# Optimization experiments

Measured on AMD Instinct MI355X. Metric: run time of the kernel, lower is better.

Reference implementation:

```python
import jax, jax.numpy as jnp
import numpy as np
from jax.scipy.special import logsumexp

# K particles, J proposal candidates, N taxa, R merges done, T current subtrees,
# S sites, A alphabet, D embedding dim
K, J, N, R, T, S, A, D = 128, 4, 64, 32, 32, 256, 4, 64
PRIOR_BL = 0.1       # expected branch length under exponential prior
TEMPERATURE = 1.0


def _gather_nodes(arr, idx):
    # arr: (Z, t, ...); idx: (Z,) -> (Z, ...)  (per-row gather, gather_K)
    i = idx.reshape((-1,) + (1,) * (arr.ndim - 1))
    return jnp.take_along_axis(arr, i, axis=1)[:, 0]


def _replace_with_merged(arr, idx1, idx2, new_val):
    # remove nodes idx1, idx2 from each row (keeping order) and append merged node
    t = arr.shape[1]
    pos = jnp.arange(t)
    removed = (pos[None, :] == idx1[:, None]) | (pos[None, :] == idx2[:, None])
    order = jnp.argsort(removed.astype(jnp.int32), axis=1, stable=True)
    kept = order[:, : t - 2]
    ki = kept.reshape(kept.shape + (1,) * (arr.ndim - 2))
    kept_vals = jnp.take_along_axis(arr, ki, axis=1)
    return jnp.concatenate([kept_vals, new_val[:, None]], axis=1)


def _hash_tree(h1, h2):
    # order-invariant int32 hash combine (wraps on overflow, as intended)
    mn = jnp.minimum(h1, h2)
    mx = jnp.maximum(h1, h2)
    return (mn * 1000003 + mx) * 40503 + 2531011


def _q_matrix(emb_ZxD, W_q):
    # GTR-style rate matrix from merged-node embedding (site-independent decoder)
    logits = (emb_ZxD @ W_q).reshape(-1, A, A)
    off = jax.nn.softplus(logits) * (1.0 - jnp.eye(A, dtype=logits.dtype))
    return off - jnp.eye(A, dtype=logits.dtype) * off.sum(-1, keepdims=True)


def setup_inputs() -> dict:
    key = jax.random.key(0)
    ks = jax.random.split(key, 20)
    merge1_indexes_Kxr = jax.random.randint(ks[0], (K, R), 0, N).astype(jnp.int32)
    merge2_indexes_Kxr = jax.random.randint(ks[1], (K, R), 0, N).astype(jnp.int32)
    branch1_lengths_Kxr = jax.random.uniform(ks[2], (K, R)) * 0.2 + 1e-3
    branch2_lengths_Kxr = jax.random.uniform(ks[3], (K, R)) * 0.2 + 1e-3
    embeddings_KxrxD = jax.random.normal(ks[4], (K, R, D))
    # leaf counts per subtree, summing to N per particle
    lc_row = jnp.concatenate([jnp.full((T // 2,), 1, jnp.int32), jnp.full((T - T // 2,), 3, jnp.int32)])
    leaf_counts_Kxt = jnp.tile(lc_row[None], (K, 1))
    hashes_Kxt = jax.random.randint(ks[5], (K, T), 0, 2 ** 30).astype(jnp.int32)
    embeddings_KxtxD = jax.random.normal(ks[6], (K, T, D))
    log_felsensteins_KxtxSxA = -jax.random.uniform(ks[7], (K, T, S, A)) * 3.0
    log_pi_K = -jax.random.uniform(ks[8], (K,)) * 100.0
    indexes_K = jax.random.randint(ks[9], (K,), 0, K).astype(jnp.int32)
    # proposal outputs (stand-in for the learned proposal): idx1 != idx2
    idx1_KxJ = jax.random.randint(ks[10], (K, J), 0, T).astype(jnp.int32)
    off = jax.random.randint(ks[11], (K, J), 1, T).astype(jnp.int32)
    idx2_KxJ = (idx1_KxJ + off) % T
    branch1_KxJ = jax.random.uniform(ks[12], (K, J)) * 0.2 + 1e-3
    branch2_KxJ = jax.random.uniform(ks[13], (K, J)) * 0.2 + 1e-3
    embedding_KxJxD = jax.random.normal(ks[14], (K, J, D))
    log_v_plus_KxJ = jnp.full((K, J), np.log(T * (T - 1) / 2.0), jnp.float32)
    gumbel_KxJ = jax.random.gumbel(ks[15], (K, J))
    W_q = jax.random.normal(ks[16], (D, A * A)) * 0.05
    W_stat = jax.random.normal(ks[17], (D, A)) * 0.05
    vals = np.zeros(2 * N, dtype=np.float64)
    for i in range(2, 2 * N):
        vals[i] = vals[i - 2] + np.log(i)
    log_double_factorials_2N = jnp.asarray(vals, jnp.float32)
    return {
        'indexes_K': indexes_K,
        'merge1_indexes_Kxr': merge1_indexes_Kxr,
        'merge2_indexes_Kxr': merge2_indexes_Kxr,
        'branch1_lengths_Kxr': branch1_lengths_Kxr,
        'branch2_lengths_Kxr': branch2_lengths_Kxr,
        'embeddings_KxrxD': embeddings_KxrxD,
        'leaf_counts_Kxt': leaf_counts_Kxt,
        'hashes_Kxt': hashes_Kxt,
        'embeddings_KxtxD': embeddings_KxtxD,
        'log_felsensteins_KxtxSxA': log_felsensteins_KxtxSxA,
        'log_pi_K': log_pi_K,
        'idx1_KxJ': idx1_KxJ,
        'idx2_KxJ': idx2_KxJ,
        'branch1_KxJ': branch1_KxJ,
        'branch2_KxJ': branch2_KxJ,
        'embedding_KxJxD': embedding_KxJxD,
        'log_v_plus_KxJ': log_v_plus_KxJ,
        'gumbel_KxJ': gumbel_KxJ,
        'W_q': W_q,
        'W_stat': W_stat,
        'log_double_factorials_2N': log_double_factorials_2N,
    }


def reference(indexes_K, merge1_indexes_Kxr, merge2_indexes_Kxr,
              branch1_lengths_Kxr, branch2_lengths_Kxr, embeddings_KxrxD,
              leaf_counts_Kxt, hashes_Kxt, embeddings_KxtxD,
              log_felsensteins_KxtxSxA, log_pi_K,
              idx1_KxJ, idx2_KxJ, branch1_KxJ, branch2_KxJ,
              embedding_KxJxD, log_v_plus_KxJ, gumbel_KxJ,
              W_q, W_stat, log_double_factorials_2N):
    # ---- ancestor resampling gather (ms[...][indexes_K]) ----
    g = lambda a: a[indexes_K]
    merge1_Kxr = g(merge1_indexes_Kxr); merge2_Kxr = g(merge2_indexes_Kxr)
    b1_Kxr = g(branch1_lengths_Kxr); b2_Kxr = g(branch2_lengths_Kxr)
    emb_KxrxD = g(embeddings_KxrxD)
    lc_Kxt = g(leaf_counts_Kxt); h_Kxt = g(hashes_Kxt)
    emb_KxtxD = g(embeddings_KxtxD)
    lf_KxtxSxA = g(log_felsensteins_KxtxSxA)
    logpi_K = g(log_pi_K)
    # ---- flatten proposal to Z = K*J (hash_trick=False: Z = K*J, no dedup) ----
    Z = K * J
    rep = lambda a: jnp.repeat(a, J, axis=0)  # K_to_Z
    idx1_Z = idx1_KxJ.reshape(Z); idx2_Z = idx2_KxJ.reshape(Z)
    branch1_Z = branch1_KxJ.reshape(Z); branch2_Z = branch2_KxJ.reshape(Z)
    emb_ZxD = embedding_KxJxD.reshape(Z, D)
    log_v_plus_Z = log_v_plus_KxJ.reshape(Z)
    merge1_Z = rep(merge1_Kxr); merge2_Z = rep(merge2_Kxr)
    b1_Z = rep(b1_Kxr); b2_Z = rep(b2_Kxr)
    embr_Z = rep(emb_KxrxD)
    lc_Z = rep(lc_Kxt); h_Z = rep(h_Kxt)
    embt_Z = rep(emb_KxtxD)
    lf_Z = rep(lf_KxtxSxA)
    logpi_Z = rep(logpi_K)
    # ---- append candidate branches ----
    b1_all = jnp.concatenate([b1_Z, branch1_Z[:, None]], axis=1)  # Z x (R+1)
    b2_all = jnp.concatenate([b2_Z, branch2_Z[:, None]], axis=1)
    # ---- merge step ----
    new_lc = _gather_nodes(lc_Z, idx1_Z) + _gather_nodes(lc_Z, idx2_Z)
    new_h = _hash_tree(_gather_nodes(h_Z, idx1_Z), _gather_nodes(h_Z, idx2_Z))
    lc_new = _replace_with_merged(lc_Z, idx1_Z, idx2_Z, new_lc)      # Z x (T-1)
    h_new = _replace_with_merged(h_Z, idx1_Z, idx2_Z, new_h)
    embt_new = _replace_with_merged(embt_Z, idx1_Z, idx2_Z, emb_ZxD)
    # ---- Felsenstein pruning update ----
    Q = _q_matrix(emb_ZxD, W_q)                                      # Z x A x A
    expm = jax.scipy.linalg.expm
    P1 = jax.vmap(expm)(Q * branch1_Z[:, None, None])
    P2 = jax.vmap(expm)(Q * branch2_Z[:, None, None])
    logP1 = jnp.log(jnp.clip(P1, 1e-30))
    logP2 = jnp.log(jnp.clip(P2, 1e-30))
    lf1 = _gather_nodes(lf_Z, idx1_Z)  # Z x S x A
    lf2 = _gather_nodes(lf_Z, idx2_Z)
    new_lf = (logsumexp(logP1[:, None, :, :] + lf1[:, :, None, :], axis=-1)
              + logsumexp(logP2[:, None, :, :] + lf2[:, :, None, :], axis=-1))
    lf_new = _replace_with_merged(lf_Z, idx1_Z, idx2_Z, new_lf)      # Z x (T-1) x S x A
    # ---- stationary probs per node & log pi ----
    log_stat = jax.nn.log_softmax(embt_new @ W_stat, axis=-1)        # Z x (T-1) x A
    ll_nodes = logsumexp(lf_new + log_stat[:, :, None, :], axis=-1).sum(-1)  # Z x (T-1)
    log_lik_Z = ll_nodes.sum(-1)
    rate = 1.0 / PRIOR_BL
    log_branch_prior = ((jnp.log(rate) - rate * b1_all).sum(-1)
                        + (jnp.log(rate) - rate * b2_all).sum(-1))
    df_idx = jnp.clip(2 * lc_new - 3, 0, 2 * N - 1)
    log_topo = -log_double_factorials_2N[df_idx].sum(-1)
    log_pi_new_Z = log_lik_Z + log_branch_prior + log_topo
    log_v_minus_Z = jnp.log(jnp.sum(lc_new > 1, axis=-1).astype(jnp.float32))
    # ---- weights & sub-resampling ----
    log_w_Z = log_pi_new_Z - logpi_Z + log_v_minus_Z - log_v_plus_Z
    log_w_KxJ = log_w_Z.reshape(K, J)
    log_weight_K = logsumexp(log_w_KxJ, axis=1) - jnp.log(float(J))
    sub_idx_K = jnp.argmax(log_w_KxJ / TEMPERATURE + gumbel_KxJ, axis=1)  # Gumbel-max = Categorical sample
    sel = jnp.arange(K) * J + sub_idx_K
    gs = lambda a: a[sel]
    merge1_out = jnp.concatenate([gs(merge1_Z), gs(idx1_Z)[:, None]], axis=1)
    merge2_out = jnp.concatenate([gs(merge2_Z), gs(idx2_Z)[:, None]], axis=1)
    embr_out = jnp.concatenate([gs(embr_Z), gs(emb_ZxD)[:, None, :]], axis=1)
    return (merge1_out, merge2_out, gs(b1_all), gs(b2_all), embr_out,
            gs(lc_new), gs(h_new), gs(embt_new), gs(lf_new),
            gs(log_pi_new_Z), log_weight_K, gs(log_lik_Z))
```

## Files before the change

### kernel.cpp

```cpp
#include <hip/hip_runtime.h>
#include <math.h>

constexpr int K_ = 128, J_ = 4, R_ = 32, T_ = 32, S_ = 256, A_ = 4, D_ = 64;
constexpr int NDF_ = 128;
constexpr float RATE_ = 10.0f;

constexpr int OFF_M1   = 0;
constexpr int OFF_M2   = OFF_M1 + K_ * 33;
constexpr int OFF_B1   = OFF_M2 + K_ * 33;
constexpr int OFF_B2   = OFF_B1 + K_ * 33;
constexpr int OFF_EMBR = OFF_B2 + K_ * 33;
constexpr int OFF_LC   = OFF_EMBR + K_ * 33 * D_;
constexpr int OFF_H    = OFF_LC + K_ * 31;
constexpr int OFF_EMBT = OFF_H + K_ * 31;
constexpr int OFF_LF   = OFF_EMBT + K_ * 31 * D_;
constexpr int OFF_LPN  = OFF_LF + K_ * 31 * S_ * A_;
constexpr int OFF_LW   = OFF_LPN + K_;
constexpr int OFF_LL   = OFF_LW + K_;

constexpr int WS_NODE  = 0;
constexpr int WS_NEWLL = WS_NODE + K_ * T_;
constexpr int WS_LOGP  = WS_NEWLL + K_ * J_;

__device__ inline float lse4f(float a, float b, float c, float d) {
    float m = fmaxf(fmaxf(a, b), fmaxf(c, d));
    return m + __logf(__expf(a - m) + __expf(b - m) + __expf(c - m) + __expf(d - m));
}

__global__ __launch_bounds__(256) void k_compute(
    const int* __restrict__ indexes, const float* __restrict__ embt,
    const float* __restrict__ lf, const float* __restrict__ Wstat,
    const float* __restrict__ Wq, const int* __restrict__ idx1_KJ,
    const int* __restrict__ idx2_KJ, const float* __restrict__ br1_KJ,
    const float* __restrict__ br2_KJ, const float* __restrict__ emb_KJD,
    float* __restrict__ ws) {
    int grp = blockIdx.x;
    int k = blockIdx.y;
    int tid = threadIdx.x, w = tid >> 6, lane = tid & 63;
    int src = indexes[k];

    if (grp < 8) {
        int t = grp * 4 + w;
        float e = embt[(src * T_ + t) * D_ + lane];
        const float4 w4 = *(const float4*)&Wstat[lane * 4];
        float g0 = e * w4.x, g1 = e * w4.y, g2 = e * w4.z, g3 = e * w4.w;
#pragma unroll
        for (int m = 32; m; m >>= 1) {
            g0 += __shfl_xor(g0, m, 64);
            g1 += __shfl_xor(g1, m, 64);
            g2 += __shfl_xor(g2, m, 64);
            g3 += __shfl_xor(g3, m, 64);
        }
        float lse = lse4f(g0, g1, g2, g3);
        float ls0 = g0 - lse, ls1 = g1 - lse, ls2 = g2 - lse, ls3 = g3 - lse;
        const float4* fr = (const float4*)&lf[(size_t)(src * T_ + t) * S_ * A_];
        double acc = 0.0;
#pragma unroll
        for (int s4 = 0; s4 < 4; ++s4) {
            float4 f = fr[s4 * 64 + lane];
            acc += (double)lse4f(f.x + ls0, f.y + ls1, f.z + ls2, f.w + ls3);
        }
#pragma unroll
        for (int m = 32; m; m >>= 1) acc += __shfl_xor(acc, m, 64);
        if (lane == 0) ws[WS_NODE + k * T_ + t] = (float)acc;
    } else {
        int z = k * J_ + w;
        int i1 = idx1_KJ[z], i2 = idx2_KJ[z];

        float emb_d = emb_KJD[z * D_ + lane];
        float lg[20];
        const float4* wqr = (const float4*)&Wq[lane * 16];
        float4 q0 = wqr[0], q1 = wqr[1], q2 = wqr[2], q3 = wqr[3];
        lg[0] = emb_d * q0.x;  lg[1] = emb_d * q0.y;  lg[2] = emb_d * q0.z;  lg[3] = emb_d * q0.w;
        lg[4] = emb_d * q1.x;  lg[5] = emb_d * q1.y;  lg[6] = emb_d * q1.z;  lg[7] = emb_d * q1.w;
        lg[8] = emb_d * q2.x;  lg[9] = emb_d * q2.y;  lg[10] = emb_d * q2.z; lg[11] = emb_d * q2.w;
        lg[12] = emb_d * q3.x; lg[13] = emb_d * q3.y; lg[14] = emb_d * q3.z; lg[15] = emb_d * q3.w;
        const float4 ws4 = *(const float4*)&Wstat[lane * 4];
        lg[16] = emb_d * ws4.x; lg[17] = emb_d * ws4.y; lg[18] = emb_d * ws4.z; lg[19] = emb_d * ws4.w;
#pragma unroll
        for (int m = 32; m; m >>= 1) {
#pragma unroll
            for (int p = 0; p < 20; ++p) lg[p] += __shfl_xor(lg[p], m, 64);
        }

        float lseS = lse4f(lg[16], lg[17], lg[18], lg[19]);
        float ls0 = lg[16] - lseS, ls1 = lg[17] - lseS, ls2 = lg[18] - lseS, ls3 = lg[19] - lseS;

        float lv[4] = {0.f, 0.f, 0.f, 0.f};
        if (lane < 8) {
            int h = lane >> 2, r = lane & 3, base = h * 4;
            float q[16];
#pragma unroll
            for (int i = 0; i < 4; ++i) {
                float rs = 0.f;
#pragma unroll
                for (int j = 0; j < 4; ++j) {
                    if (i != j) {
                        float x = lg[i * 4 + j];
                        float sp = (x > 15.f) ? x : log1pf(__expf(x));
                        q[i * 4 + j] = sp;
                        rs += sp;
                    }
                }
                q[i * 4 + i] = -rs;
            }
            float br = (h == 0) ? br1_KJ[z] : br2_KJ[z];
            float c = br * (1.f / 64.f);
#pragma unroll
            for (int e2 = 0; e2 < 16; ++e2) q[e2] *= c;
            float trow[4], arow[4];
#pragma unroll
            for (int j = 0; j < 4; ++j) { trow[j] = (j == r) ? 1.f : 0.f; arow[j] = trow[j]; }
            const float inv_n[11] = {0.f, 1.f, 0.5f, 1.f / 3.f, 0.25f, 0.2f,
                                     1.f / 6.f, 1.f / 7.f, 0.125f, 1.f / 9.f, 0.1f};
#pragma unroll
            for (int n = 1; n <= 10; ++n) {
                float nt[4];
#pragma unroll
                for (int j = 0; j < 4; ++j)
                    nt[j] = (trow[0] * q[0 * 4 + j] + trow[1] * q[1 * 4 + j] +
                             trow[2] * q[2 * 4 + j] + trow[3] * q[3 * 4 + j]) * inv_n[n];
#pragma unroll
                for (int j = 0; j < 4; ++j) { trow[j] = nt[j]; arow[j] += nt[j]; }
            }
#pragma unroll
            for (int sq = 0; sq < 6; ++sq) {
                float nrow[4];
#pragma unroll
                for (int j = 0; j < 4; ++j) {
                    float aj = arow[j];
                    nrow[j] = arow[0] * __shfl(aj, base + 0, 64)
                            + arow[1] * __shfl(aj, base + 1, 64)
                            + arow[2] * __shfl(aj, base + 2, 64)
                            + arow[3] * __shfl(aj, base + 3, 64);
                }
#pragma unroll
                for (int j = 0; j < 4; ++j) arow[j] = nrow[j];
            }
#pragma unroll
            for (int j = 0; j < 4; ++j) {
                lv[j] = __logf(fmaxf(arow[j], 1e-30f));
                ws[WS_LOGP + z * 32 + h * 16 + r * 4 + j] = lv[j];
            }
        }
        float p1[16], p2[16];
#pragma unroll
        for (int r = 0; r < 4; ++r) {
#pragma unroll
            for (int j = 0; j < 4; ++j) {
                p1[r * 4 + j] = __shfl(lv[j], r, 64);
                p2[r * 4 + j] = __shfl(lv[j], 4 + r, 64);
            }
        }
        const float4* f1p = (const float4*)&lf[(size_t)(src * T_ + i1) * S_ * A_];
        const float4* f2p = (const float4*)&lf[(size_t)(src * T_ + i2) * S_ * A_];
        double acc = 0.0;
#pragma unroll
        for (int s4 = 0; s4 < 4; ++s4) {
            float4 f = f1p[s4 * 64 + lane];
            float4 f2v = f2p[s4 * 64 + lane];
            float nlf[4];
#pragma unroll
            for (int a = 0; a < 4; ++a) {
                float t1 = lse4f(p1[a * 4 + 0] + f.x, p1[a * 4 + 1] + f.y,
                                 p1[a * 4 + 2] + f.z, p1[a * 4 + 3] + f.w);
                float t2 = lse4f(p2[a * 4 + 0] + f2v.x, p2[a * 4 + 1] + f2v.y,
                                 p2[a * 4 + 2] + f2v.z, p2[a * 4 + 3] + f2v.w);
                nlf[a] = t1 + t2;
            }
            acc += (double)lse4f(nlf[0] + ls0, nlf[1] + ls1, nlf[2] + ls2, nlf[3] + ls3);
        }
#pragma unroll
        for (int m = 32; m; m >>= 1) acc += __shfl_xor(acc, m, 64);
        if (lane == 0) ws[WS_NEWLL + z] = (float)acc;
    }
}

__global__ __launch_bounds__(256) void k_out(
    const int* __restrict__ indexes, const int* __restrict__ m1_Kr,
    const int* __restrict__ m2_Kr, const float* __restrict__ b1_Kr,
    const float* __restrict__ b2_Kr, const float* __restrict__ embr,
    const int* __restrict__ lc_Kt, const int* __restrict__ h_Kt,
    const float* __restrict__ embt, const float* __restrict__ lf,
    const float* __restrict__ logpi_K, const int* __restrict__ idx1_KJ,
    const int* __restrict__ idx2_KJ, const float* __restrict__ br1_KJ,
    const float* __restrict__ br2_KJ, const float* __restrict__ emb_KJD,
    const float* __restrict__ logvp_KJ, const float* __restrict__ gumbel_KJ,
    const float* __restrict__ ldf, const float* __restrict__ ws,
    float* __restrict__ out) {
    int grp = blockIdx.x;
    int k = blockIdx.y;
    int tid = threadIdx.x, lane = tid & 63;
    int src = indexes[k];

    double nll = 0.0, topo = 0.0, sb1 = 0.0, sb2 = 0.0;
    int cnt = 0;
    if (lane < T_) {
        nll = (double)ws[WS_NODE + k * T_ + lane];
        int lc = lc_Kt[src * T_ + lane];
        int di = 2 * lc - 3; di = max(0, min(NDF_ - 1, di));
        topo = (double)ldf[di];
        cnt = (lc > 1) ? 1 : 0;
        sb1 = (double)b1_Kr[src * R_ + lane];
        sb2 = (double)b2_Kr[src * R_ + lane];
    }
#pragma unroll
    for (int m = 32; m; m >>= 1) {
        nll += __shfl_xor(nll, m, 64);
        topo += __shfl_xor(topo, m, 64);
        sb1 += __shfl_xor(sb1, m, 64);
        sb2 += __shfl_xor(sb2, m, 64);
        cnt += __shfl_xor(cnt, m, 64);
    }
    double total_ll = nll, base_topo = -topo;
    const double lr = log(10.0);

    double lwj = 0.0, lpnj = 0.0, llikj = 0.0, scorej = -1.0e300;
    if (lane < J_) {
        int j = lane, z = k * J_ + j;
        int i1 = idx1_KJ[z], i2 = idx2_KJ[z];
        int lc1 = lc_Kt[src * T_ + i1], lc2 = lc_Kt[src * T_ + i2];
        int nlc = lc1 + lc2;
        double loglik = total_ll - (double)ws[WS_NODE + k * T_ + i1]
                      - (double)ws[WS_NODE + k * T_ + i2] + (double)ws[WS_NEWLL + z];
        double lbp = 66.0 * lr
                   - (double)RATE_ * (sb1 + (double)br1_KJ[z] + sb2 + (double)br2_KJ[z]);
        int d1 = max(0, min(NDF_ - 1, 2 * lc1 - 3));
        int d2 = max(0, min(NDF_ - 1, 2 * lc2 - 3));
        int dn = max(0, min(NDF_ - 1, 2 * nlc - 3));
        double lt = base_topo + (double)ldf[d1] + (double)ldf[d2] - (double)ldf[dn];
        int cntj = cnt - ((lc1 > 1) ? 1 : 0) - ((lc2 > 1) ? 1 : 0) + 1;
        double lvm = log((double)cntj);
        lpnj = loglik + lbp + lt;
        llikj = loglik;
        lwj = lpnj - (double)logpi_K[src] + lvm - (double)logvp_KJ[z];
        scorej = lwj + (double)gumbel_KJ[z];
    }
    double lw0 = __shfl(lwj, 0, 64), lw1 = __shfl(lwj, 1, 64);
    double lw2 = __shfl(lwj, 2, 64), lw3 = __shfl(lwj, 3, 64);
    double sc0 = __shfl(scorej, 0, 64), sc1 = __shfl(scorej, 1, 64);
    double sc2 = __shfl(scorej, 2, 64), sc3 = __shfl(scorej, 3, 64);
    int best = 0;
    double bv = sc0;
    if (sc1 > bv) { bv = sc1; best = 1; }
    if (sc2 > bv) { bv = sc2; best = 2; }
    if (sc3 > bv) { bv = sc3; best = 3; }
    int zs = k * J_ + best;
    int si1 = idx1_KJ[zs], si2 = idx2_KJ[zs];
    int mn = min(si1, si2), mx = max(si1, si2);

    if (grp < 8) {
        __shared__ float sP[32];
        if (grp == 7) {
            if (tid < 32) sP[tid] = ws[WS_LOGP + zs * 32 + tid];
            __syncthreads();
        }
#pragma unroll
        for (int rr = 0; rr < 4; ++rr) {
            int row = grp * 4 + rr;
            if (row >= 31) break;
            if (row < 30) {
                int st = row;
                if (st >= mn) ++st;
                if (st >= mx) ++st;
                const float4 v = *(const float4*)&lf[((size_t)(src * T_ + st) * S_ + tid) * A_];
                *(float4*)&out[OFF_LF + ((size_t)(k * 31 + row) * S_ + tid) * A_] = v;
            } else {
                float P1[16], P2[16];
#pragma unroll
                for (int i = 0; i < 16; ++i) { P1[i] = sP[i]; P2[i] = sP[16 + i]; }
                const float4 f1 = *(const float4*)&lf[((size_t)(src * T_ + si1) * S_ + tid) * A_];
                const float4 f2 = *(const float4*)&lf[((size_t)(src * T_ + si2) * S_ + tid) * A_];
                float4 o4;
#pragma unroll
                for (int a = 0; a < 4; ++a) {
                    float t1 = lse4f(P1[a * 4 + 0] + f1.x, P1[a * 4 + 1] + f1.y,
                                     P1[a * 4 + 2] + f1.z, P1[a * 4 + 3] + f1.w);
                    float t2 = lse4f(P2[a * 4 + 0] + f2.x, P2[a * 4 + 1] + f2.y,
                                     P2[a * 4 + 2] + f2.z, P2[a * 4 + 3] + f2.w);
                    ((float*)&o4)[a] = t1 + t2;
                }
                *(float4*)&out[OFF_LF + ((size_t)(k * 31 + 30) * S_ + tid) * A_] = o4;
            }
        }
    } else {
        if (tid == 0) {
            double m = fmax(fmax(lw0, lw1), fmax(lw2, lw3));
            double ssum = exp(lw0 - m) + exp(lw1 - m) + exp(lw2 - m) + exp(lw3 - m);
            double logw = m + log(ssum) - log((double)J_);
            out[OFF_LW + k] = (float)logw;
        }
        double lpn_b = __shfl(lpnj, best, 64);
        double llik_b = __shfl(llikj, best, 64);
        if (tid == 0) {
            out[OFF_LPN + k] = (float)lpn_b;
            out[OFF_LL + k] = (float)llik_b;
        }
        for (int i = tid; i < 33; i += 256) {
            float v1, v2, fb1, fb2;
            if (i < 32) {
                v1 = (float)m1_Kr[src * R_ + i];
                v2 = (float)m2_Kr[src * R_ + i];
                fb1 = b1_Kr[src * R_ + i];
                fb2 = b2_Kr[src * R_ + i];
            } else {
                v1 = (float)si1; v2 = (float)si2;
                fb1 = br1_KJ[zs]; fb2 = br2_KJ[zs];
            }
            out[OFF_M1 + k * 33 + i] = v1;
            out[OFF_M2 + k * 33 + i] = v2;
            out[OFF_B1 + k * 33 + i] = fb1;
            out[OFF_B2 + k * 33 + i] = fb2;
        }
        for (int i = tid; i < 31; i += 256) {
            int lcv, hv;
            if (i < 30) {
                int st = i;
                if (st >= mn) ++st;
                if (st >= mx) ++st;
                lcv = lc_Kt[src * T_ + st];
                hv = h_Kt[src * T_ + st];
            } else {
                lcv = lc_Kt[src * T_ + si1] + lc_Kt[src * T_ + si2];
                int h1 = h_Kt[src * T_ + si1], h2 = h_Kt[src * T_ + si2];
                int hmn = min(h1, h2), hmx = max(h1, h2);
                unsigned int u = ((unsigned int)hmn * 1000003u + (unsigned int)hmx) * 40503u
                                 + 2531011u;
                hv = (int)u;
            }
            out[OFF_LC + k * 31 + i] = (float)lcv;
            out[OFF_H + k * 31 + i] = (float)hv;
        }
        for (int i = tid; i < 33 * 16; i += 256) {
            int r = i >> 4, c = i & 15;
            float4 v = (r < 32) ? *(const float4*)&embr[(src * R_ + r) * D_ + c * 4]
                                : *(const float4*)&emb_KJD[zs * D_ + c * 4];
            *(float4*)&out[OFF_EMBR + k * 33 * D_ + i * 4] = v;
        }
        for (int i = tid; i < 31 * 16; i += 256) {
            int t = i >> 4, c = i & 15;
            float4 v;
            if (t < 30) {
                int st = t;
                if (st >= mn) ++st;
                if (st >= mx) ++st;
                v = *(const float4*)&embt[(src * T_ + st) * D_ + c * 4];
            } else {
                v = *(const float4*)&emb_KJD[zs * D_ + c * 4];
            }
            *(float4*)&out[OFF_EMBT + k * 31 * D_ + i * 4] = v;
        }
    }
}

extern "C" void kernel_launch(void* const* d_in, const int* in_sizes, int n_in,
                              void* d_out, int out_size, void* d_ws, size_t ws_size,
                              hipStream_t stream) {
    const int* indexes   = (const int*)d_in[0];
    const int* m1_Kr     = (const int*)d_in[1];
    const int* m2_Kr     = (const int*)d_in[2];
    const float* b1_Kr   = (const float*)d_in[3];
    const float* b2_Kr   = (const float*)d_in[4];
    const float* embr    = (const float*)d_in[5];
    const int* lc_Kt     = (const int*)d_in[6];
    const int* h_Kt      = (const int*)d_in[7];
    const float* embt    = (const float*)d_in[8];
    const float* lf      = (const float*)d_in[9];
    const float* logpi_K = (const float*)d_in[10];
    const int* idx1_KJ   = (const int*)d_in[11];
    const int* idx2_KJ   = (const int*)d_in[12];
    const float* br1_KJ  = (const float*)d_in[13];
    const float* br2_KJ  = (const float*)d_in[14];
    const float* emb_KJD = (const float*)d_in[15];
    const float* logvp_KJ = (const float*)d_in[16];
    const float* gumbel_KJ = (const float*)d_in[17];
    const float* Wq      = (const float*)d_in[18];
    const float* Wstat   = (const float*)d_in[19];
    const float* ldf     = (const float*)d_in[20];
    float* out = (float*)d_out;
    float* ws = (float*)d_ws;

    k_compute<<<dim3(9, K_), 256, 0, stream>>>(indexes, embt, lf, Wstat, Wq,
                                               idx1_KJ, idx2_KJ, br1_KJ, br2_KJ,
                                               emb_KJD, ws);
    k_out<<<dim3(9, K_), 256, 0, stream>>>(indexes, m1_Kr, m2_Kr, b1_Kr, b2_Kr,
                                           embr, lc_Kt, h_Kt, embt, lf, logpi_K,
                                           idx1_KJ, idx2_KJ, br1_KJ, br2_KJ,
                                           emb_KJD, logvp_KJ, gumbel_KJ, ldf,
                                           ws, out);
}
```

Before: 132.0 us.

## Fuse compute and output kernels with per-particle atomic counter barrier

Merges the compute and output kernels into one launch. The 9 blocks of each particle synchronise through an atomic counter in workspace that a memset clears before the launch. This removes the kernel boundary and second launch, but adds a spin-wait barrier that relies on all blocks of a particle being co-resident. It also adds a memset operation and shifts the workspace offsets.

```diff
diff --git a/kernel.cpp b/kernel.cpp
--- a/kernel.cpp
+++ b/kernel.cpp
@@ -4,6 +4,7 @@
 constexpr int K_ = 128, J_ = 4, R_ = 32, T_ = 32, S_ = 256, A_ = 4, D_ = 64;
 constexpr int NDF_ = 128;
 constexpr float RATE_ = 10.0f;
+constexpr int GRPS_ = 9;
 
 constexpr int OFF_M1   = 0;
 constexpr int OFF_M2   = OFF_M1 + K_ * 33;
@@ -18,7 +19,7 @@
 constexpr int OFF_LW   = OFF_LPN + K_;
 constexpr int OFF_LL   = OFF_LW + K_;
 
-constexpr int WS_NODE  = 0;
+constexpr int WS_NODE  = 2048;
 constexpr int WS_NEWLL = WS_NODE + K_ * T_;
 constexpr int WS_LOGP  = WS_NEWLL + K_ * J_;
 
@@ -27,13 +28,19 @@
     return m + __logf(__expf(a - m) + __expf(b - m) + __expf(c - m) + __expf(d - m));
 }
 
-__global__ __launch_bounds__(256) void k_compute(
-    const int* __restrict__ indexes, const float* __restrict__ embt,
-    const float* __restrict__ lf, const float* __restrict__ Wstat,
-    const float* __restrict__ Wq, const int* __restrict__ idx1_KJ,
+__global__ __launch_bounds__(256, 5) void k_fused(
+    const int* __restrict__ indexes, const int* __restrict__ m1_Kr,
+    const int* __restrict__ m2_Kr, const float* __restrict__ b1_Kr,
+    const float* __restrict__ b2_Kr, const float* __restrict__ embr,
+    const int* __restrict__ lc_Kt, const int* __restrict__ h_Kt,
+    const float* __restrict__ embt, const float* __restrict__ lf,
+    const float* __restrict__ logpi_K, const int* __restrict__ idx1_KJ,
     const int* __restrict__ idx2_KJ, const float* __restrict__ br1_KJ,
     const float* __restrict__ br2_KJ, const float* __restrict__ emb_KJD,
-    float* __restrict__ ws) {
+    const float* __restrict__ logvp_KJ, const float* __restrict__ gumbel_KJ,
+    const float* __restrict__ Wq, const float* __restrict__ Wstat,
+    const float* __restrict__ ldf, float* __restrict__ ws,
+    float* __restrict__ out) {
     int grp = blockIdx.x;
     int k = blockIdx.y;
     int tid = threadIdx.x, w = tid >> 6, lane = tid & 63;
@@ -174,24 +181,18 @@
         for (int m = 32; m; m >>= 1) acc += __shfl_xor(acc, m, 64);
         if (lane == 0) ws[WS_NEWLL + z] = (float)acc;
     }
-}
-
-__global__ __launch_bounds__(256) void k_out(
-    const int* __restrict__ indexes, const int* __restrict__ m1_Kr,
-    const int* __restrict__ m2_Kr, const float* __restrict__ b1_Kr,
-    const float* __restrict__ b2_Kr, const float* __restrict__ embr,
-    const int* __restrict__ lc_Kt, const int* __restrict__ h_Kt,
-    const float* __restrict__ embt, const float* __restrict__ lf,
-    const float* __restrict__ logpi_K, const int* __restrict__ idx1_KJ,
-    const int* __restrict__ idx2_KJ, const float* __restrict__ br1_KJ,
-    const float* __restrict__ br2_KJ, const float* __restrict__ emb_KJD,
-    const float* __restrict__ logvp_KJ, const float* __restrict__ gumbel_KJ,
-    const float* __restrict__ ldf, const float* __restrict__ ws,
-    float* __restrict__ out) {
-    int grp = blockIdx.x;
-    int k = blockIdx.y;
-    int tid = threadIdx.x, lane = tid & 63;
-    int src = indexes[k];
+
+    {
+        volatile int* ctr = (volatile int*)ws + (size_t)k * 16;
+        __threadfence();
+        __syncthreads();
+        if (tid == 0) {
+            atomicAdd((int*)ctr, 1);
+            while (*ctr < GRPS_) __builtin_amdgcn_s_sleep(16);
+        }
+        __syncthreads();
+        __threadfence();
+    }
 
     double nll = 0.0, topo = 0.0, sb1 = 0.0, sb2 = 0.0;
     int cnt = 0;
@@ -380,12 +381,9 @@
     float* out = (float*)d_out;
     float* ws = (float*)d_ws;
 
-    k_compute<<<dim3(9, K_), 256, 0, stream>>>(indexes, embt, lf, Wstat, Wq,
-                                               idx1_KJ, idx2_KJ, br1_KJ, br2_KJ,
-                                               emb_KJD, ws);
-    k_out<<<dim3(9, K_), 256, 0, stream>>>(indexes, m1_Kr, m2_Kr, b1_Kr, b2_Kr,
-                                           embr, lc_Kt, h_Kt, embt, lf, logpi_K,
-                                           idx1_KJ, idx2_KJ, br1_KJ, br2_KJ,
-                                           emb_KJD, logvp_KJ, gumbel_KJ, ldf,
-                                           ws, out);
+    hipMemsetAsync(d_ws, 0, 8192, stream);
+    k_fused<<<dim3(GRPS_, K_), 256, 0, stream>>>(
+        indexes, m1_Kr, m2_Kr, b1_Kr, b2_Kr, embr, lc_Kt, h_Kt, embt, lf,
+        logpi_K, idx1_KJ, idx2_KJ, br1_KJ, br2_KJ, emb_KJD, logvp_KJ,
+        gumbel_KJ, Wq, Wstat, ldf, ws, out);
 }
```

After: 294.9 us. +123.4%, slower.
